# Kernel tuning notes

Hardware: AMD Instinct MI355X
Metric: run time of the kernel (lower is better)

The kernel has to match this reference:

```python
import jax, jax.numpy as jnp
import numpy as np

B, G, K, C, NT = 128, 64, 32, 256, 8192


def setup_inputs() -> dict:
    key = jax.random.key(0)
    ks = jax.random.split(key, 8)
    s = lambda fan_in: 1.0 / np.sqrt(fan_in)
    return {
        "patch_features": jax.random.normal(ks[0], (B, G, C), jnp.float32),
        "neighborhood": jax.random.normal(ks[1], (B, G, K, 3), jnp.float32),
        "codebook": jax.random.normal(ks[2], (NT, C), jnp.float32),
        "w1": jax.random.normal(ks[3], (512, C), jnp.float32) * s(C),
        "b1": jnp.zeros((512,), jnp.float32),
        "w2": jax.random.normal(ks[4], (256, 512), jnp.float32) * s(512),
        "b2": jnp.zeros((256,), jnp.float32),
        "w3": jax.random.normal(ks[5], (3 * K, 256), jnp.float32) * s(256),
        "b3": jnp.zeros((3 * K,), jnp.float32),
    }


def reference(patch_features, neighborhood, codebook, w1, b1, w2, b2, w3, b3):
    b, g, c = patch_features.shape
    k = neighborhood.shape[2]
    # squared euclidean distances to codebook (argmin equals argmin of cdist p=2)
    d2 = (
        jnp.sum(patch_features * patch_features, -1, keepdims=True)
        - 2.0 * jnp.einsum("bgc,nc->bgn", patch_features, codebook)
        + jnp.sum(codebook * codebook, -1)
    )  # [B,G,NT]
    token_ids = jnp.argmin(d2, axis=-1)          # [B,G]
    quantized = codebook[token_ids]              # [B,G,C] gather
    # 1x1 Conv1d stack == per-token MLP
    h = jax.nn.relu(jnp.einsum("bgc,oc->bgo", quantized, w1) + b1)
    h = jax.nn.relu(jnp.einsum("bgc,oc->bgo", h, w2) + b2)
    rec = jnp.einsum("bgc,oc->bgo", h, w3) + b3  # [B,G,3K]
    rec = rec.reshape(b * g, k, 3)
    gt = neighborhood.reshape(b * g, k, 3)
    # Chamfer distance L2 (squared) both directions
    diff = rec[:, :, None, :] - gt[:, None, :, :]  # [BG,K,K,3]
    dd = jnp.sum(diff * diff, -1)                  # [BG,K,K]
    loss = jnp.mean(jnp.min(dd, axis=2)) + jnp.mean(jnp.min(dd, axis=1))
    return loss
```

## Files before the change

kernel.cpp:

```cpp
#include <hip/hip_runtime.h>
#include <hip/hip_bf16.h>
#include <float.h>

#define NTOK 8192
#define NCB  8192
#define CDIM 256
#define KPTS 32
#define SQNT 24.0f
#define INV_CFOLD (SQNT * SQNT * 64.0f)

#define CG   4
#define NTPB 16

typedef __attribute__((ext_vector_type(8))) short short8;
typedef __attribute__((ext_vector_type(4))) float f32x4;
typedef __attribute__((ext_vector_type(4))) int i32x4;
typedef __attribute__((ext_vector_type(16))) int i32x16;
typedef unsigned int u32;
typedef unsigned long long u64;

__device__ __forceinline__ void gl_lds16(const void* g, void* l) {
  __builtin_amdgcn_global_load_lds(
      (const __attribute__((address_space(1))) u32*)(g),
      (__attribute__((address_space(3))) u32*)(l), 16, 0, 0);
}

__device__ __forceinline__ ushort bf16_rne(float x) {
  u32 u = __float_as_uint(x);
  return (ushort)((u + 0x7fffu + ((u >> 16) & 1u)) >> 16);
}

__device__ __forceinline__ int pack4i8(int a, int b, int c, int d) {
  return (a & 0xff) | ((b & 0xff) << 8) | ((c & 0xff) << 16) | ((d & 0xff) << 24);
}

__global__ __launch_bounds__(256) void prep_k(
    const float* __restrict__ pf, const float* __restrict__ cb,
    const float* __restrict__ w1, const float* __restrict__ w2,
    const float* __restrict__ w3,
    i32x4* __restrict__ pf1, i32x4* __restrict__ pf2,
    i32x4* __restrict__ cb1, i32x4* __restrict__ cb2,
    ushort* __restrict__ cb_bf, ushort* __restrict__ w1s,
    ushort* __restrict__ w2s, ushort* __restrict__ w3s,
    float* __restrict__ cnorm, float* __restrict__ out) {
  __shared__ float cred[4][16];
  if (blockIdx.x == 0 && threadIdx.x == 0) out[0] = 0.f;
  int gid = blockIdx.x * 4 + (threadIdx.x >> 6);
  int wv = threadIdx.x >> 6;
  int lane = threadIdx.x & 63, r16 = lane & 15, quad = lane >> 4;
  if (gid < 4096) {
    bool is_cb = gid >= 2048;
    int t = is_cb ? gid - 2048 : gid;
    int tile = t >> 2, kb = t & 3;
    const float* src = is_cb ? cb : pf;
    int row = tile * 16 + r16;
    const float* sp = src + (size_t)row * CDIM + kb * 64 + quad * 16;
    float4 v0 = ((const float4*)sp)[0];
    float4 v1 = ((const float4*)sp)[1];
    float4 v2 = ((const float4*)sp)[2];
    float4 v3 = ((const float4*)sp)[3];
    float x[16] = {v0.x, v0.y, v0.z, v0.w, v1.x, v1.y, v1.z, v1.w,
                   v2.x, v2.y, v2.z, v2.w, v3.x, v3.y, v3.z, v3.w};
    int q1[16], q2[16];
    float s = 0.f;
#pragma unroll
    for (int e = 0; e < 16; e++) {
      float as = x[e] * SQNT;
      float a1 = rintf(as);
      a1 = fminf(fmaxf(a1, -127.f), 127.f);
      float a2 = rintf((as - a1) * 128.f);
      a2 = fminf(fmaxf(a2, -127.f), 127.f);
      q1[e] = (int)a1;
      q2[e] = (int)a2;
      s += x[e] * x[e];
    }
    i32x4 p1 = {pack4i8(q1[0], q1[1], q1[2], q1[3]),
                pack4i8(q1[4], q1[5], q1[6], q1[7]),
                pack4i8(q1[8], q1[9], q1[10], q1[11]),
                pack4i8(q1[12], q1[13], q1[14], q1[15])};
    i32x4 p2 = {pack4i8(q2[0], q2[1], q2[2], q2[3]),
                pack4i8(q2[4], q2[5], q2[6], q2[7]),
                pack4i8(q2[8], q2[9], q2[10], q2[11]),
                pack4i8(q2[12], q2[13], q2[14], q2[15])};
    int rt32 = tile >> 1;
    int row_in = ((tile & 1) << 4) | r16;
    int kc32 = (kb << 1) | (quad >> 1);
    int k_half = quad & 1;
    size_t o = (size_t)(rt32 * 8 + kc32) * 64 + k_half * 32 + row_in;
    (is_cb ? cb1 : pf1)[o] = p1;
    (is_cb ? cb2 : pf2)[o] = p2;
    if (is_cb) {
      int kb32 = 2 * kb + (quad >> 1);
      int slot0 = ((2 * quad) & 3) * 16 + r16;
      int slot1 = ((2 * quad + 1) & 3) * 16 + r16;
      size_t bo = ((size_t)tile * 8 + kb32) * 512;
      short8 vh0 = {(short)bf16_rne(x[0]), (short)bf16_rne(x[1]),
                    (short)bf16_rne(x[2]), (short)bf16_rne(x[3]),
                    (short)bf16_rne(x[4]), (short)bf16_rne(x[5]),
                    (short)bf16_rne(x[6]), (short)bf16_rne(x[7])};
      short8 vh1 = {(short)bf16_rne(x[8]), (short)bf16_rne(x[9]),
                    (short)bf16_rne(x[10]), (short)bf16_rne(x[11]),
                    (short)bf16_rne(x[12]), (short)bf16_rne(x[13]),
                    (short)bf16_rne(x[14]), (short)bf16_rne(x[15])};
      *(short8*)(cb_bf + bo + (size_t)slot0 * 8) = vh0;
      *(short8*)(cb_bf + bo + (size_t)slot1 * 8) = vh1;
      s += __shfl_xor(s, 16, 64);
      s += __shfl_xor(s, 32, 64);
      if (quad == 0) cred[wv][r16] = s;
      __syncthreads();
      if (threadIdx.x < 16) {
        int ctile = blockIdx.x - 512;
        cnorm[ctile * 16 + threadIdx.x] =
            cred[0][threadIdx.x] + cred[1][threadIdx.x] +
            cred[2][threadIdx.x] + cred[3][threadIdx.x];
      }
    }
  } else if (gid < 4656) {
    int t = gid - 4096;
    const float* src;
    ushort* dst;
    int KB;
    if (t < 256)      { src = w1; dst = w1s; KB = 8; }
    else if (t < 512) { src = w2; dst = w2s; KB = 16; t -= 256; }
    else              { src = w3; dst = w3s; KB = 8;  t -= 512; }
    int tile = t / KB, kb = t - tile * KB, K = KB * 32;
    int row = tile * 16 + r16;
    const float* sp = src + (size_t)row * K + kb * 32 + quad * 8;
    float4 a = ((const float4*)sp)[0];
    float4 b = ((const float4*)sp)[1];
    short8 vh = {(short)bf16_rne(a.x), (short)bf16_rne(a.y),
                 (short)bf16_rne(a.z), (short)bf16_rne(a.w),
                 (short)bf16_rne(b.x), (short)bf16_rne(b.y),
                 (short)bf16_rne(b.z), (short)bf16_rne(b.w)};
    *(short8*)(dst + ((size_t)tile * KB + kb) * 512 + lane * 8) = vh;
  }
}

__device__ __forceinline__ void stage_b(const char* __restrict__ B1g,
                                        const char* __restrict__ B2g,
                                        size_t ctb, int kh, char* dst,
                                        int wv, int lane) {
#pragma unroll
  for (int u = 0; u < 8; ++u) {
    int c = wv * 8 + u;
    int lv = c >> 4, ct = (c >> 2) & 3, kc = (c & 3) + kh * 4;
    const char* src = (lv ? B2g : B1g) +
                      ((ctb + ct) * 8 + kc) * 1024 + (size_t)lane * 16;
    gl_lds16(src, dst + c * 1024);
  }
}

template <int KH>
__device__ __forceinline__ void phase_mfma(const char* bcur, int wc, int lane,
                                           const i32x4* a1, const i32x4* a2,
                                           i32x16* am, i32x16* ac) {
#pragma unroll
  for (int kk = 0; kk < 4; ++kk) {
#pragma unroll
    for (int j = 0; j < 2; ++j) {
      int ct = wc * 2 + j;
      i32x4 b1 = *(const i32x4*)(bcur + (ct * 4 + kk) * 1024 + lane * 16);
      i32x4 b2 = *(const i32x4*)(bcur + (16 + ct * 4 + kk) * 1024 + lane * 16);
      am[j] = __builtin_amdgcn_mfma_i32_32x32x32_i8(a1[KH * 4 + kk], b1, am[j], 0, 0, 0);
      ac[j] = __builtin_amdgcn_mfma_i32_32x32x32_i8(a1[KH * 4 + kk], b2, ac[j], 0, 0, 0);
      ac[j] = __builtin_amdgcn_mfma_i32_32x32x32_i8(a2[KH * 4 + kk], b1, ac[j], 0, 0, 0);
    }
  }
}

__global__ __launch_bounds__(256, 2) void argmin_k(
    const char* __restrict__ A1g, const char* __restrict__ A2g,
    const char* __restrict__ B1g, const char* __restrict__ B2g,
    const float* __restrict__ cnorm, u64* __restrict__ pkeys) {
  extern __shared__ char lds[];
  char* buf0 = lds;
  char* buf1 = lds + 32768;
  int tid = threadIdx.x;
  int cg = blockIdx.x, mt = blockIdx.y;
  int wv = tid >> 6, lane = tid & 63;
  int rt = wv >> 1, wc = wv & 1;
  int l31 = lane & 31, lh = lane >> 5;

  i32x4 a1[8], a2[8];
  {
    int rtg = mt * 2 + rt;
    const char* a1p = A1g + (size_t)rtg * 8192 + (size_t)lane * 16;
    const char* a2p = A2g + (size_t)rtg * 8192 + (size_t)lane * 16;
#pragma unroll
    for (int kc = 0; kc < 8; ++kc) {
      a1[kc] = *(const i32x4*)(a1p + kc * 1024);
      a2[kc] = *(const i32x4*)(a2p + kc * 1024);
    }
#pragma unroll
    for (int kc = 0; kc < 8; ++kc) {
      asm volatile("" : "+v"(a1[kc]));
      asm volatile("" : "+v"(a2[kc]));
    }
  }

  stage_b(B1g, B2g, (size_t)(cg * NTPB) * 4, 0, buf0, wv, lane);
  __syncthreads();

  int bvi[16], bii[16];
#pragma unroll
  for (int r = 0; r < 16; ++r) { bvi[r] = 0x7fffffff; bii[r] = 0x7fffffff; }

  i32x16 am[2], ac[2];

  for (int n = 0; n < NTPB; ++n) {
    size_t ctb = (size_t)(cg * NTPB + n) * 4;
    stage_b(B1g, B2g, ctb, 1, buf1, wv, lane);
#pragma unroll
    for (int j = 0; j < 2; ++j)
#pragma unroll
      for (int r = 0; r < 16; ++r) { am[j][r] = 0; ac[j][r] = 0; }
    phase_mfma<0>(buf0, wc, lane, a1, a2, am, ac);
    __syncthreads();
    if (n + 1 < NTPB) stage_b(B1g, B2g, ctb + 4, 0, buf0, wv, lane);
    phase_mfma<1>(buf1, wc, lane, a1, a2, am, ac);
    {
      int colbase = (cg * NTPB + n) * 128 + wc * 64;
#pragma unroll
      for (int j = 0; j < 2; ++j) {
        int col = colbase + j * 32 + l31;
        int cni = __float2int_rn(cnorm[col] * INV_CFOLD);
#pragma unroll
        for (int r = 0; r < 16; ++r) {
          int di = cni - (am[j][r] * 128 + ac[j][r]);
          if (di < bvi[r]) { bvi[r] = di; bii[r] = col; }
        }
      }
    }
    __syncthreads();
  }

#pragma unroll
  for (int m = 1; m < 32; m <<= 1) {
#pragma unroll
    for (int r = 0; r < 16; ++r) {
      int ov = __shfl_xor(bvi[r], m, 64);
      int oi = __shfl_xor(bii[r], m, 64);
      if (ov < bvi[r] || (ov == bvi[r] && oi < bii[r])) {
        bvi[r] = ov;
        bii[r] = oi;
      }
    }
  }
  if (l31 == 0) {
    int rowb = mt * 64 + rt * 32 + 4 * lh;
    size_t sbase = (size_t)(cg * 2 + wc) * NTOK;
#pragma unroll
    for (int r = 0; r < 16; ++r) {
      int row = rowb + (r & 3) + 8 * (r >> 2);
      u32 mk = (u32)(bvi[r] + (1 << 30));
      pkeys[sbase + row] = ((u64)mk << 32) | (u32)bii[r];
    }
  }
}

__global__ __launch_bounds__(512) void mlp_fused_k(
    const u64* __restrict__ pkeys, const ushort* __restrict__ cb_bf,
    const ushort* __restrict__ w1s, const float* __restrict__ b1,
    const ushort* __restrict__ w2s, const float* __restrict__ b2,
    const ushort* __restrict__ w3s, const float* __restrict__ b3,
    const float* __restrict__ neigh, float* __restrict__ out) {
  __shared__ ushort qs_h2[8 * 512];
  __shared__ ushort h1s[16 * 512];
  __shared__ float rec[16 * 96];
  __shared__ float gts[16 * 96];
  __shared__ int ids[16];
  __shared__ float wsum[8];

  int tid = threadIdx.x;
  int t0 = blockIdx.x * 16;
  int wv = tid >> 6, lane = tid & 63;
  int quad = lane >> 4, r16 = lane & 15;

  if (tid < 128) {
    int row_l = tid >> 3, sl = tid & 7;
    u64 best = pkeys[(size_t)sl * NTOK + t0 + row_l];
#pragma unroll
    for (int m = 1; m < 8; m <<= 1) {
      u64 o = __shfl_xor((unsigned long long)best, m, 64);
      if (o < best) best = o;
    }
    if (sl == 0) ids[row_l] = (int)(u32)best;
  }
  __syncthreads();

  {
    int kb = wv;
    int id = ids[r16];
    short8 v = *(const short8*)(cb_bf + ((size_t)(id >> 4) * 8 + kb) * 512 +
                                (size_t)((id & 15) + quad * 16) * 8);
    *(short8*)(qs_h2 + (size_t)kb * 512 + lane * 8) = v;
  }
  __syncthreads();

  short8 fa1[8];
#pragma unroll
  for (int kb = 0; kb < 8; kb++)
    fa1[kb] = *(const short8*)(qs_h2 + (size_t)kb * 512 + lane * 8);
  __syncthreads();

#pragma unroll
  for (int jj = 0; jj < 4; ++jj) {
    int jt = wv + jj * 8;
    f32x4 acc = (f32x4){0.f, 0.f, 0.f, 0.f};
#pragma unroll
    for (int kb = 0; kb < 8; kb++) {
      short8 fb = *(const short8*)(w1s + ((size_t)jt * 8 + kb) * 512 + lane * 8);
      acc = __builtin_amdgcn_mfma_f32_16x16x32_bf16(fa1[kb], fb, acc, 0, 0, 0);
    }
    int col = jt * 16 + r16;
    float bj = b1[col];
#pragma unroll
    for (int reg = 0; reg < 4; reg++) {
      int row_l = quad * 4 + reg;
      float v = fmaxf(acc[reg] + bj, 0.f);
      size_t o = (size_t)(col >> 5) * 512 +
                 (size_t)(((col >> 3) & 3) * 16 + row_l) * 8 + (col & 7);
      h1s[o] = bf16_rne(v);
    }
  }
  __syncthreads();

#pragma unroll
  for (int jj = 0; jj < 2; ++jj) {
    int jt = wv + jj * 8;
    f32x4 acc = (f32x4){0.f, 0.f, 0.f, 0.f};
#pragma unroll
    for (int kb = 0; kb < 16; kb++) {
      short8 fa = *(const short8*)(h1s + (size_t)kb * 512 + lane * 8);
      short8 fb = *(const short8*)(w2s + ((size_t)jt * 16 + kb) * 512 + lane * 8);
      acc = __builtin_amdgcn_mfma_f32_16x16x32_bf16(fa, fb, acc, 0, 0, 0);
    }
    int col = jt * 16 + r16;
    float bj = b2[col];
#pragma unroll
    for (int reg = 0; reg < 4; reg++) {
      int row_l = quad * 4 + reg;
      float v = fmaxf(acc[reg] + bj, 0.f);
      size_t o = (size_t)(col >> 5) * 512 +
                 (size_t)(((col >> 3) & 3) * 16 + row_l) * 8 + (col & 7);
      qs_h2[o] = bf16_rne(v);
    }
  }
  __syncthreads();

  if (tid < 384) {
    int t = tid / 24, c = (tid - t * 24) * 4;
    *(float4*)(gts + (size_t)t * 96 + c) =
        *(const float4*)(neigh + (size_t)(t0 + t) * 96 + c);
  }

  if (wv < 6) {
    int jt = wv;
    f32x4 acc = (f32x4){0.f, 0.f, 0.f, 0.f};
#pragma unroll
    for (int kb = 0; kb < 8; kb++) {
      short8 fa = *(const short8*)(qs_h2 + (size_t)kb * 512 + lane * 8);
      short8 fb = *(const short8*)(w3s + ((size_t)jt * 8 + kb) * 512 + lane * 8);
      acc = __builtin_amdgcn_mfma_f32_16x16x32_bf16(fa, fb, acc, 0, 0, 0);
    }
    int col = jt * 16 + r16;
    float bj = b3[col];
#pragma unroll
    for (int reg = 0; reg < 4; reg++) {
      int row_l = quad * 4 + reg;
      rec[(size_t)row_l * 96 + col] = acc[reg] + bj;
    }
  }
  __syncthreads();

  float local = 0.f;
  {
    int t = tid >> 5, i = tid & 31;
    float rx = rec[t * 96 + 3 * i], ry = rec[t * 96 + 3 * i + 1], rz = rec[t * 96 + 3 * i + 2];
    float gx = gts[t * 96 + 3 * i], gy = gts[t * 96 + 3 * i + 1], gz = gts[t * 96 + 3 * i + 2];
    float mA = FLT_MAX, mB = FLT_MAX;
#pragma unroll
    for (int j = 0; j < 32; j++) {
      float dx = rx - gts[t * 96 + 3 * j], dy = ry - gts[t * 96 + 3 * j + 1],
            dz = rz - gts[t * 96 + 3 * j + 2];
      float d = dx * dx + dy * dy + dz * dz;
      mA = fminf(mA, d);
      dx = rec[t * 96 + 3 * j] - gx; dy = rec[t * 96 + 3 * j + 1] - gy;
      dz = rec[t * 96 + 3 * j + 2] - gz;
      d = dx * dx + dy * dy + dz * dz;
      mB = fminf(mB, d);
    }
    local = mA + mB;
  }
#pragma unroll
  for (int off = 32; off; off >>= 1) local += __shfl_down(local, off, 64);
  if (lane == 0) wsum[wv] = local;
  __syncthreads();
  if (tid == 0) {
    float s = 0.f;
#pragma unroll
    for (int w = 0; w < 8; w++) s += wsum[w];
    atomicAdd(out, s * (1.0f / (float)(NTOK * KPTS)));
  }
}

extern "C" void kernel_launch(void* const* d_in, const int* in_sizes, int n_in,
                              void* d_out, int out_size, void* d_ws, size_t ws_size,
                              hipStream_t stream) {
  const float* pf    = (const float*)d_in[0];
  const float* neigh = (const float*)d_in[1];
  const float* cb    = (const float*)d_in[2];
  const float* w1    = (const float*)d_in[3];
  const float* b1    = (const float*)d_in[4];
  const float* w2    = (const float*)d_in[5];
  const float* b2    = (const float*)d_in[6];
  const float* w3    = (const float*)d_in[7];
  const float* b3    = (const float*)d_in[8];
  float* out = (float*)d_out;
  char* base = (char*)d_ws;

  u64*   pkeys = (u64*)base;
  float* cnorm = (float*)(base + 0x200000);
  char*  pf1   = base + 0x210000;
  char*  pf2   = base + 0x410000;
  char*  cb1   = base + 0x610000;
  char*  cb2   = base + 0x810000;
  ushort* cb_bf = (ushort*)(base + 0xA10000);
  ushort* w1s   = (ushort*)(base + 0xE10000);
  ushort* w2s   = (ushort*)(base + 0xE50000);
  ushort* w3s   = (ushort*)(base + 0xE90000);

  prep_k<<<1164, 256, 0, stream>>>(pf, cb, w1, w2, w3,
                                   (i32x4*)pf1, (i32x4*)pf2, (i32x4*)cb1,
                                   (i32x4*)cb2, cb_bf, w1s, w2s, w3s, cnorm, out);
  argmin_k<<<dim3(CG, 128), 256, 65536, stream>>>(pf1, pf2, cb1, cb2, cnorm, pkeys);
  mlp_fused_k<<<512, 512, 0, stream>>>(pkeys, cb_bf, w1s, b1, w2s, b2,
                                       w3s, b3, neigh, out);
}
```

Baseline: 162.8 us.

## Replace double-buffered B staging with 4-slot quarter-tile ring and vmcnt waits

Restructures the argmin GEMM's codebook staging from two 32KB halves with __syncthreads into a 4-slot ring of 16KB quarter-tiles, prefetched two phases ahead. It uses explicit s_waitcnt vmcnt counts with a single s_barrier per phase, so loads stay in flight across barriers instead of being fully drained. It also raises wave priority around the MFMA block. This trades finer-grained barriers (four per tile instead of two) and hand-tuned wait counts for better overlap of global-to-LDS copies with MFMA work.

Measured after the change: 164.5 us. Within noise of the previous version (+1.0%).

```diff
diff --git a/kernel.cpp b/kernel.cpp
--- a/kernel.cpp
+++ b/kernel.cpp
@@ -136,34 +136,70 @@
   }
 }
 
-__device__ __forceinline__ void stage_b(const char* __restrict__ B1g,
-                                        const char* __restrict__ B2g,
-                                        size_t ctb, int kh, char* dst,
-                                        int wv, int lane) {
-#pragma unroll
-  for (int u = 0; u < 8; ++u) {
-    int c = wv * 8 + u;
-    int lv = c >> 4, ct = (c >> 2) & 3, kc = (c & 3) + kh * 4;
-    const char* src = (lv ? B2g : B1g) +
-                      ((ctb + ct) * 8 + kc) * 1024 + (size_t)lane * 16;
-    gl_lds16(src, dst + c * 1024);
-  }
-}
-
-template <int KH>
-__device__ __forceinline__ void phase_mfma(const char* bcur, int wc, int lane,
-                                           const i32x4* a1, const i32x4* a2,
-                                           i32x16* am, i32x16* ac) {
-#pragma unroll
-  for (int kk = 0; kk < 4; ++kk) {
+__device__ __forceinline__ void stage_half(const char* __restrict__ B1g,
+                                           const char* __restrict__ B2g,
+                                           int cg, int G, char* dst,
+                                           int wv, int lane) {
+  int n_g = G >> 2, h_g = G & 3;
+  const char* base = ((wv & 2) ? B2g : B1g) +
+                     ((size_t)(cg * NTPB + n_g) << 15) + (size_t)lane * 16;
+#pragma unroll
+  for (int u = 0; u < 4; ++u) {
+    int ct = (wv & 1) * 2 + (u >> 1);
+    int kp = h_g * 2 + (u & 1);
+    int c  = (wv >> 1) * 8 + ct * 2 + (u & 1);
+    gl_lds16(base + ct * 8192 + kp * 1024, dst + c * 1024);
+  }
+}
+
+template <int HL, int VN, bool STG>
+__device__ __forceinline__ void phase(
+    const char* __restrict__ B1g, const char* __restrict__ B2g,
+    char* lds, int cg, int n, int wv, int wc, int lane, int l31,
+    const i32x4* a1, const i32x4* a2, i32x16* am, i32x16* ac,
+    const float* __restrict__ cnorm, int* bvi, int* bii) {
+  constexpr int SLOT = HL & 3;
+  constexpr int TSLOT = (HL + 2) & 3;
+  if constexpr (STG)
+    stage_half(B1g, B2g, cg, n * 4 + HL + 2, lds + TSLOT * 16384, wv, lane);
+  if constexpr (HL == 0) {
+#pragma unroll
+    for (int j = 0; j < 2; ++j)
+#pragma unroll
+      for (int r = 0; r < 16; ++r) { am[j][r] = 0; ac[j][r] = 0; }
+  }
+  if constexpr (VN == 8)      asm volatile("s_waitcnt vmcnt(8)" ::: "memory");
+  else if constexpr (VN == 4) asm volatile("s_waitcnt vmcnt(4)" ::: "memory");
+  else                        asm volatile("s_waitcnt vmcnt(0)" ::: "memory");
+  __builtin_amdgcn_s_barrier();
+  __builtin_amdgcn_sched_barrier(0);
+  const char* sb = lds + SLOT * 16384 + (size_t)lane * 16;
+  __builtin_amdgcn_s_setprio(1);
+#pragma unroll
+  for (int kcl = 0; kcl < 2; ++kcl) {
+    const int kp = HL * 2 + kcl;
 #pragma unroll
     for (int j = 0; j < 2; ++j) {
       int ct = wc * 2 + j;
-      i32x4 b1 = *(const i32x4*)(bcur + (ct * 4 + kk) * 1024 + lane * 16);
-      i32x4 b2 = *(const i32x4*)(bcur + (16 + ct * 4 + kk) * 1024 + lane * 16);
-      am[j] = __builtin_amdgcn_mfma_i32_32x32x32_i8(a1[KH * 4 + kk], b1, am[j], 0, 0, 0);
-      ac[j] = __builtin_amdgcn_mfma_i32_32x32x32_i8(a1[KH * 4 + kk], b2, ac[j], 0, 0, 0);
-      ac[j] = __builtin_amdgcn_mfma_i32_32x32x32_i8(a2[KH * 4 + kk], b1, ac[j], 0, 0, 0);
+      i32x4 b1 = *(const i32x4*)(sb + (ct * 2 + kcl) * 1024);
+      i32x4 b2 = *(const i32x4*)(sb + (8 + ct * 2 + kcl) * 1024);
+      am[j] = __builtin_amdgcn_mfma_i32_32x32x32_i8(a1[kp], b1, am[j], 0, 0, 0);
+      ac[j] = __builtin_amdgcn_mfma_i32_32x32x32_i8(a1[kp], b2, ac[j], 0, 0, 0);
+      ac[j] = __builtin_amdgcn_mfma_i32_32x32x32_i8(a2[kp], b1, ac[j], 0, 0, 0);
+    }
+  }
+  __builtin_amdgcn_s_setprio(0);
+  if constexpr (HL == 3) {
+    int colbase = (cg * NTPB + n) * 128 + wc * 64;
+#pragma unroll
+    for (int j = 0; j < 2; ++j) {
+      int col = colbase + j * 32 + l31;
+      int cni = __float2int_rn(cnorm[col] * INV_CFOLD);
+#pragma unroll
+      for (int r = 0; r < 16; ++r) {
+        int di = cni - (am[j][r] * 128 + ac[j][r]);
+        if (di < bvi[r]) { bvi[r] = di; bii[r] = col; }
+      }
     }
   }
 }
@@ -173,8 +209,6 @@
     const char* __restrict__ B1g, const char* __restrict__ B2g,
     const float* __restrict__ cnorm, u64* __restrict__ pkeys) {
   extern __shared__ char lds[];
-  char* buf0 = lds;
-  char* buf1 = lds + 32768;
   int tid = threadIdx.x;
   int cg = blockIdx.x, mt = blockIdx.y;
   int wv = tid >> 6, lane = tid & 63;
@@ -198,8 +232,8 @@
     }
   }
 
-  stage_b(B1g, B2g, (size_t)(cg * NTPB) * 4, 0, buf0, wv, lane);
-  __syncthreads();
+  stage_half(B1g, B2g, cg, 0, lds, wv, lane);
+  stage_half(B1g, B2g, cg, 1, lds + 16384, wv, lane);
 
   int bvi[16], bii[16];
 #pragma unroll
@@ -207,31 +241,18 @@
 
   i32x16 am[2], ac[2];
 
-  for (int n = 0; n < NTPB; ++n) {
-    size_t ctb = (size_t)(cg * NTPB + n) * 4;
-    stage_b(B1g, B2g, ctb, 1, buf1, wv, lane);
-#pragma unroll
-    for (int j = 0; j < 2; ++j)
-#pragma unroll
-      for (int r = 0; r < 16; ++r) { am[j][r] = 0; ac[j][r] = 0; }
-    phase_mfma<0>(buf0, wc, lane, a1, a2, am, ac);
-    __syncthreads();
-    if (n + 1 < NTPB) stage_b(B1g, B2g, ctb + 4, 0, buf0, wv, lane);
-    phase_mfma<1>(buf1, wc, lane, a1, a2, am, ac);
-    {
-      int colbase = (cg * NTPB + n) * 128 + wc * 64;
-#pragma unroll
-      for (int j = 0; j < 2; ++j) {
-        int col = colbase + j * 32 + l31;
-        int cni = __float2int_rn(cnorm[col] * INV_CFOLD);
-#pragma unroll
-        for (int r = 0; r < 16; ++r) {
-          int di = cni - (am[j][r] * 128 + ac[j][r]);
-          if (di < bvi[r]) { bvi[r] = di; bii[r] = col; }
-        }
-      }
-    }
-    __syncthreads();
+  for (int n = 0; n < NTPB - 1; ++n) {
+    phase<0, 8, true>(B1g, B2g, lds, cg, n, wv, wc, lane, l31, a1, a2, am, ac, cnorm, bvi, bii);
+    phase<1, 8, true>(B1g, B2g, lds, cg, n, wv, wc, lane, l31, a1, a2, am, ac, cnorm, bvi, bii);
+    phase<2, 8, true>(B1g, B2g, lds, cg, n, wv, wc, lane, l31, a1, a2, am, ac, cnorm, bvi, bii);
+    phase<3, 8, true>(B1g, B2g, lds, cg, n, wv, wc, lane, l31, a1, a2, am, ac, cnorm, bvi, bii);
+  }
+  {
+    const int n = NTPB - 1;
+    phase<0, 8, true >(B1g, B2g, lds, cg, n, wv, wc, lane, l31, a1, a2, am, ac, cnorm, bvi, bii);
+    phase<1, 8, true >(B1g, B2g, lds, cg, n, wv, wc, lane, l31, a1, a2, am, ac, cnorm, bvi, bii);
+    phase<2, 4, false>(B1g, B2g, lds, cg, n, wv, wc, lane, l31, a1, a2, am, ac, cnorm, bvi, bii);
+    phase<3, 0, false>(B1g, B2g, lds, cg, n, wv, wc, lane, l31, a1, a2, am, ac, cnorm, bvi, bii);
   }
 
 #pragma unroll
```

## Split argmin codebook across more blocks with narrower tiles and MFMA priority

Applied to the files above, without the earlier changes.

The codebook sweep is split into 16 column groups instead of 4. Each block now handles 64-column tiles instead of 128, so each wave keeps one accumulator pair rather than two. The LDS double buffer is halved, which allows three blocks per CU, and the MFMA loops are wrapped in s_setprio. The MLP kernel now reduces 32 partial argmin keys per token instead of 8. The aim is more blocks and more occupancy to hide load latency, at the cost of more partial-result writes and a larger final reduction.

Result: slower. 172.4 us (+5.9%).

```diff
diff --git a/kernel.cpp b/kernel.cpp
--- a/kernel.cpp
+++ b/kernel.cpp
@@ -9,8 +9,8 @@
 #define SQNT 24.0f
 #define INV_CFOLD (SQNT * SQNT * 64.0f)
 
-#define CG   4
-#define NTPB 16
+#define CG   16
+#define NTPB 8
 
 typedef __attribute__((ext_vector_type(8))) short short8;
 typedef __attribute__((ext_vector_type(4))) float f32x4;
@@ -136,45 +136,27 @@
   }
 }
 
-__device__ __forceinline__ void stage_b(const char* __restrict__ B1g,
-                                        const char* __restrict__ B2g,
-                                        size_t ctb, int kh, char* dst,
-                                        int wv, int lane) {
-#pragma unroll
-  for (int u = 0; u < 8; ++u) {
-    int c = wv * 8 + u;
-    int lv = c >> 4, ct = (c >> 2) & 3, kc = (c & 3) + kh * 4;
+__device__ __forceinline__ void stage_ph(const char* __restrict__ B1g,
+                                         const char* __restrict__ B2g,
+                                         int ctb , int kh,
+                                         char* dst, int wv, int lane) {
+#pragma unroll
+  for (int u = 0; u < 4; ++u) {
+    int c = wv * 4 + u;
+    int lv = c >> 3, ct = (c >> 2) & 1, kcl = c & 3;
     const char* src = (lv ? B2g : B1g) +
-                      ((ctb + ct) * 8 + kc) * 1024 + (size_t)lane * 16;
+        ((size_t)(ctb + ct) * 8 + kh * 4 + kcl) * 1024 + (size_t)lane * 16;
     gl_lds16(src, dst + c * 1024);
   }
 }
 
-template <int KH>
-__device__ __forceinline__ void phase_mfma(const char* bcur, int wc, int lane,
-                                           const i32x4* a1, const i32x4* a2,
-                                           i32x16* am, i32x16* ac) {
-#pragma unroll
-  for (int kk = 0; kk < 4; ++kk) {
-#pragma unroll
-    for (int j = 0; j < 2; ++j) {
-      int ct = wc * 2 + j;
-      i32x4 b1 = *(const i32x4*)(bcur + (ct * 4 + kk) * 1024 + lane * 16);
-      i32x4 b2 = *(const i32x4*)(bcur + (16 + ct * 4 + kk) * 1024 + lane * 16);
-      am[j] = __builtin_amdgcn_mfma_i32_32x32x32_i8(a1[KH * 4 + kk], b1, am[j], 0, 0, 0);
-      ac[j] = __builtin_amdgcn_mfma_i32_32x32x32_i8(a1[KH * 4 + kk], b2, ac[j], 0, 0, 0);
-      ac[j] = __builtin_amdgcn_mfma_i32_32x32x32_i8(a2[KH * 4 + kk], b1, ac[j], 0, 0, 0);
-    }
-  }
-}
-
-__global__ __launch_bounds__(256, 2) void argmin_k(
+__global__ __launch_bounds__(256, 3) void argmin_k(
     const char* __restrict__ A1g, const char* __restrict__ A2g,
     const char* __restrict__ B1g, const char* __restrict__ B2g,
     const float* __restrict__ cnorm, u64* __restrict__ pkeys) {
   extern __shared__ char lds[];
   char* buf0 = lds;
-  char* buf1 = lds + 32768;
+  char* buf1 = lds + 16384;
   int tid = threadIdx.x;
   int cg = blockIdx.x, mt = blockIdx.y;
   int wv = tid >> 6, lane = tid & 63;
@@ -198,37 +180,55 @@
     }
   }
 
-  stage_b(B1g, B2g, (size_t)(cg * NTPB) * 4, 0, buf0, wv, lane);
+  stage_ph(B1g, B2g, cg * NTPB * 2, 0, buf0, wv, lane);
   __syncthreads();
 
   int bvi[16], bii[16];
 #pragma unroll
   for (int r = 0; r < 16; ++r) { bvi[r] = 0x7fffffff; bii[r] = 0x7fffffff; }
 
-  i32x16 am[2], ac[2];
+  i32x16 am, ac;
 
   for (int n = 0; n < NTPB; ++n) {
-    size_t ctb = (size_t)(cg * NTPB + n) * 4;
-    stage_b(B1g, B2g, ctb, 1, buf1, wv, lane);
-#pragma unroll
-    for (int j = 0; j < 2; ++j)
-#pragma unroll
-      for (int r = 0; r < 16; ++r) { am[j][r] = 0; ac[j][r] = 0; }
-    phase_mfma<0>(buf0, wc, lane, a1, a2, am, ac);
+    int ctb = (cg * NTPB + n) * 2;
+    stage_ph(B1g, B2g, ctb, 1, buf1, wv, lane);
+#pragma unroll
+    for (int r = 0; r < 16; ++r) { am[r] = 0; ac[r] = 0; }
+    {
+      const char* sb = buf0 + (size_t)(wc * 4) * 1024 + (size_t)lane * 16;
+      __builtin_amdgcn_s_setprio(1);
+#pragma unroll
+      for (int kc = 0; kc < 4; ++kc) {
+        i32x4 b1 = *(const i32x4*)(sb + kc * 1024);
+        i32x4 b2 = *(const i32x4*)(sb + 8192 + kc * 1024);
+        am = __builtin_amdgcn_mfma_i32_32x32x32_i8(a1[kc], b1, am, 0, 0, 0);
+        ac = __builtin_amdgcn_mfma_i32_32x32x32_i8(a1[kc], b2, ac, 0, 0, 0);
+        ac = __builtin_amdgcn_mfma_i32_32x32x32_i8(a2[kc], b1, ac, 0, 0, 0);
+      }
+      __builtin_amdgcn_s_setprio(0);
+    }
     __syncthreads();
-    if (n + 1 < NTPB) stage_b(B1g, B2g, ctb + 4, 0, buf0, wv, lane);
-    phase_mfma<1>(buf1, wc, lane, a1, a2, am, ac);
+    if (n + 1 < NTPB) stage_ph(B1g, B2g, ctb + 2, 0, buf0, wv, lane);
     {
-      int colbase = (cg * NTPB + n) * 128 + wc * 64;
-#pragma unroll
-      for (int j = 0; j < 2; ++j) {
-        int col = colbase + j * 32 + l31;
-        int cni = __float2int_rn(cnorm[col] * INV_CFOLD);
-#pragma unroll
-        for (int r = 0; r < 16; ++r) {
-          int di = cni - (am[j][r] * 128 + ac[j][r]);
-          if (di < bvi[r]) { bvi[r] = di; bii[r] = col; }
-        }
+      const char* sb = buf1 + (size_t)(wc * 4) * 1024 + (size_t)lane * 16;
+      __builtin_amdgcn_s_setprio(1);
+#pragma unroll
+      for (int kc = 0; kc < 4; ++kc) {
+        i32x4 b1 = *(const i32x4*)(sb + kc * 1024);
+        i32x4 b2 = *(const i32x4*)(sb + 8192 + kc * 1024);
+        am = __builtin_amdgcn_mfma_i32_32x32x32_i8(a1[4 + kc], b1, am, 0, 0, 0);
+        ac = __builtin_amdgcn_mfma_i32_32x32x32_i8(a1[4 + kc], b2, ac, 0, 0, 0);
+        ac = __builtin_amdgcn_mfma_i32_32x32x32_i8(a2[4 + kc], b1, ac, 0, 0, 0);
+      }
+      __builtin_amdgcn_s_setprio(0);
+    }
+    {
+      int col = (cg * NTPB + n) * 64 + wc * 32 + l31;
+      int cni = __float2int_rn(cnorm[col] * INV_CFOLD);
+#pragma unroll
+      for (int r = 0; r < 16; ++r) {
+        int di = cni - (am[r] * 128 + ac[r]);
+        if (di < bvi[r]) { bvi[r] = di; bii[r] = col; }
       }
     }
     __syncthreads();
@@ -276,11 +276,11 @@
   int wv = tid >> 6, lane = tid & 63;
   int quad = lane >> 4, r16 = lane & 15;
 
-  if (tid < 128) {
-    int row_l = tid >> 3, sl = tid & 7;
+  {
+    int row_l = tid >> 5, sl = tid & 31;
     u64 best = pkeys[(size_t)sl * NTOK + t0 + row_l];
 #pragma unroll
-    for (int m = 1; m < 8; m <<= 1) {
+    for (int m = 1; m < 32; m <<= 1) {
       u64 o = __shfl_xor((unsigned long long)best, m, 64);
       if (o < best) best = o;
     }
@@ -433,7 +433,7 @@
   prep_k<<<1164, 256, 0, stream>>>(pf, cb, w1, w2, w3,
                                    (i32x4*)pf1, (i32x4*)pf2, (i32x4*)cb1,
                                    (i32x4*)cb2, cb_bf, w1s, w2s, w3s, cnorm, out);
-  argmin_k<<<dim3(CG, 128), 256, 65536, stream>>>(pf1, pf2, cb1, cb2, cnorm, pkeys);
+  argmin_k<<<dim3(CG, 128), 256, 32768, stream>>>(pf1, pf2, cb1, cb2, cnorm, pkeys);
   mlp_fused_k<<<512, 512, 0, stream>>>(pkeys, cb_bf, w1s, b1, w2s, b2,
                                        w3s, b3, neigh, out);
 }
```

## Stream codebook tiles directly into registers in argmin, dropping LDS staging

Applied to the files above, without the earlier changes.

Rewrites the int8 MFMA argmin kernel so each wave owns one 32-row token tile and loads codebook fragments straight from global memory into double-buffered registers. This replaces the shared-memory staging and the per-iteration block barriers. Codebook norms are now precomputed once per block into LDS, and the grid becomes 8 column groups by 64 row groups. The cost is that the four waves of a block each fetch the same codebook data separately, which raises L2/global traffic and makes the loop more sensitive to memory latency.

Measured after the change: 166.9 us. 1.02x slower.

```diff
diff --git a/kernel.cpp b/kernel.cpp
--- a/kernel.cpp
+++ b/kernel.cpp
@@ -9,8 +9,8 @@
 #define SQNT 24.0f
 #define INV_CFOLD (SQNT * SQNT * 64.0f)
 
-#define CG   4
-#define NTPB 16
+#define CG   8
+#define TW   32
 
 typedef __attribute__((ext_vector_type(8))) short short8;
 typedef __attribute__((ext_vector_type(4))) float f32x4;
@@ -18,12 +18,6 @@
 typedef __attribute__((ext_vector_type(16))) int i32x16;
 typedef unsigned int u32;
 typedef unsigned long long u64;
-
-__device__ __forceinline__ void gl_lds16(const void* g, void* l) {
-  __builtin_amdgcn_global_load_lds(
-      (const __attribute__((address_space(1))) u32*)(g),
-      (__attribute__((address_space(3))) u32*)(l), 16, 0, 0);
-}
 
 __device__ __forceinline__ ushort bf16_rne(float x) {
   u32 u = __float_as_uint(x);
@@ -136,35 +130,24 @@
   }
 }
 
-__device__ __forceinline__ void stage_b(const char* __restrict__ B1g,
-                                        const char* __restrict__ B2g,
-                                        size_t ctb, int kh, char* dst,
-                                        int wv, int lane) {
-#pragma unroll
-  for (int u = 0; u < 8; ++u) {
-    int c = wv * 8 + u;
-    int lv = c >> 4, ct = (c >> 2) & 3, kc = (c & 3) + kh * 4;
-    const char* src = (lv ? B2g : B1g) +
-                      ((ctb + ct) * 8 + kc) * 1024 + (size_t)lane * 16;
-    gl_lds16(src, dst + c * 1024);
-  }
-}
-
-template <int KH>
-__device__ __forceinline__ void phase_mfma(const char* bcur, int wc, int lane,
-                                           const i32x4* a1, const i32x4* a2,
-                                           i32x16* am, i32x16* ac) {
-#pragma unroll
-  for (int kk = 0; kk < 4; ++kk) {
-#pragma unroll
-    for (int j = 0; j < 2; ++j) {
-      int ct = wc * 2 + j;
-      i32x4 b1 = *(const i32x4*)(bcur + (ct * 4 + kk) * 1024 + lane * 16);
-      i32x4 b2 = *(const i32x4*)(bcur + (16 + ct * 4 + kk) * 1024 + lane * 16);
-      am[j] = __builtin_amdgcn_mfma_i32_32x32x32_i8(a1[KH * 4 + kk], b1, am[j], 0, 0, 0);
-      ac[j] = __builtin_amdgcn_mfma_i32_32x32x32_i8(a1[KH * 4 + kk], b2, ac[j], 0, 0, 0);
-      ac[j] = __builtin_amdgcn_mfma_i32_32x32x32_i8(a2[KH * 4 + kk], b1, ac[j], 0, 0, 0);
-    }
+__device__ __forceinline__ void loadh(const char* bb1, const char* bb2,
+                                      int offb, i32x4 (&q1)[4], i32x4 (&q2)[4]) {
+#pragma unroll
+  for (int k = 0; k < 4; ++k) {
+    q1[k] = *(const i32x4*)(bb1 + (size_t)(offb + k) * 1024);
+    q2[k] = *(const i32x4*)(bb2 + (size_t)(offb + k) * 1024);
+  }
+}
+
+template <int KB>
+__device__ __forceinline__ void mfmah(const i32x4* a1, const i32x4* a2,
+                                      const i32x4 (&q1)[4], const i32x4 (&q2)[4],
+                                      i32x16& am, i32x16& ac) {
+#pragma unroll
+  for (int k = 0; k < 4; ++k) {
+    am = __builtin_amdgcn_mfma_i32_32x32x32_i8(a1[KB + k], q1[k], am, 0, 0, 0);
+    ac = __builtin_amdgcn_mfma_i32_32x32x32_i8(a1[KB + k], q2[k], ac, 0, 0, 0);
+    ac = __builtin_amdgcn_mfma_i32_32x32x32_i8(a2[KB + k], q1[k], ac, 0, 0, 0);
   }
 }
 
@@ -172,18 +155,18 @@
     const char* __restrict__ A1g, const char* __restrict__ A2g,
     const char* __restrict__ B1g, const char* __restrict__ B2g,
     const float* __restrict__ cnorm, u64* __restrict__ pkeys) {
-  extern __shared__ char lds[];
-  char* buf0 = lds;
-  char* buf1 = lds + 32768;
+  __shared__ int cni_lds[1024];
   int tid = threadIdx.x;
   int cg = blockIdx.x, mt = blockIdx.y;
   int wv = tid >> 6, lane = tid & 63;
-  int rt = wv >> 1, wc = wv & 1;
   int l31 = lane & 31, lh = lane >> 5;
+
+  for (int k = tid; k < 1024; k += 256)
+    cni_lds[k] = __float2int_rn(cnorm[cg * 1024 + k] * INV_CFOLD);
 
   i32x4 a1[8], a2[8];
   {
-    int rtg = mt * 2 + rt;
+    int rtg = mt * 4 + wv;
     const char* a1p = A1g + (size_t)rtg * 8192 + (size_t)lane * 16;
     const char* a2p = A2g + (size_t)rtg * 8192 + (size_t)lane * 16;
 #pragma unroll
@@ -197,41 +180,49 @@
       asm volatile("" : "+v"(a2[kc]));
     }
   }
-
-  stage_b(B1g, B2g, (size_t)(cg * NTPB) * 4, 0, buf0, wv, lane);
   __syncthreads();
 
   int bvi[16], bii[16];
 #pragma unroll
   for (int r = 0; r < 16; ++r) { bvi[r] = 0x7fffffff; bii[r] = 0x7fffffff; }
 
-  i32x16 am[2], ac[2];
-
-  for (int n = 0; n < NTPB; ++n) {
-    size_t ctb = (size_t)(cg * NTPB + n) * 4;
-    stage_b(B1g, B2g, ctb, 1, buf1, wv, lane);
-#pragma unroll
-    for (int j = 0; j < 2; ++j)
-#pragma unroll
-      for (int r = 0; r < 16; ++r) { am[j][r] = 0; ac[j][r] = 0; }
-    phase_mfma<0>(buf0, wc, lane, a1, a2, am, ac);
-    __syncthreads();
-    if (n + 1 < NTPB) stage_b(B1g, B2g, ctb + 4, 0, buf0, wv, lane);
-    phase_mfma<1>(buf1, wc, lane, a1, a2, am, ac);
-    {
-      int colbase = (cg * NTPB + n) * 128 + wc * 64;
-#pragma unroll
-      for (int j = 0; j < 2; ++j) {
-        int col = colbase + j * 32 + l31;
-        int cni = __float2int_rn(cnorm[col] * INV_CFOLD);
-#pragma unroll
-        for (int r = 0; r < 16; ++r) {
-          int di = cni - (am[j][r] * 128 + ac[j][r]);
-          if (di < bvi[r]) { bvi[r] = di; bii[r] = col; }
-        }
-      }
-    }
-    __syncthreads();
+  const char* bb1 = B1g + (size_t)(cg * TW) * 8192 + (size_t)lane * 16;
+  const char* bb2 = B2g + (size_t)(cg * TW) * 8192 + (size_t)lane * 16;
+
+  i32x4 q1A[4], q2A[4], q1B[4], q2B[4];
+  i32x16 am, ac;
+
+  loadh(bb1, bb2, 0, q1A, q2A);
+  loadh(bb1, bb2, 4, q1B, q2B);
+
+  for (int t = 0; t < TW - 1; ++t) {
+#pragma unroll
+    for (int r = 0; r < 16; ++r) { am[r] = 0; ac[r] = 0; }
+    mfmah<0>(a1, a2, q1A, q2A, am, ac);
+    loadh(bb1, bb2, (t + 1) * 8, q1A, q2A);
+    mfmah<4>(a1, a2, q1B, q2B, am, ac);
+    loadh(bb1, bb2, (t + 1) * 8 + 4, q1B, q2B);
+    int cni = cni_lds[t * 32 + l31];
+    int col = cg * 1024 + t * 32 + l31;
+#pragma unroll
+    for (int r = 0; r < 16; ++r) {
+      int di = cni - (am[r] * 128 + ac[r]);
+      if (di < bvi[r]) { bvi[r] = di; bii[r] = col; }
+    }
+  }
+  {
+    const int t = TW - 1;
+#pragma unroll
+    for (int r = 0; r < 16; ++r) { am[r] = 0; ac[r] = 0; }
+    mfmah<0>(a1, a2, q1A, q2A, am, ac);
+    mfmah<4>(a1, a2, q1B, q2B, am, ac);
+    int cni = cni_lds[t * 32 + l31];
+    int col = cg * 1024 + t * 32 + l31;
+#pragma unroll
+    for (int r = 0; r < 16; ++r) {
+      int di = cni - (am[r] * 128 + ac[r]);
+      if (di < bvi[r]) { bvi[r] = di; bii[r] = col; }
+    }
   }
 
 #pragma unroll
@@ -247,8 +238,8 @@
     }
   }
   if (l31 == 0) {
-    int rowb = mt * 64 + rt * 32 + 4 * lh;
-    size_t sbase = (size_t)(cg * 2 + wc) * NTOK;
+    int rowb = mt * 128 + wv * 32 + 4 * lh;
+    size_t sbase = (size_t)cg * NTOK;
 #pragma unroll
     for (int r = 0; r < 16; ++r) {
       int row = rowb + (r & 3) + 8 * (r >> 2);
@@ -433,7 +424,7 @@
   prep_k<<<1164, 256, 0, stream>>>(pf, cb, w1, w2, w3,
                                    (i32x4*)pf1, (i32x4*)pf2, (i32x4*)cb1,
                                    (i32x4*)cb2, cb_bf, w1s, w2s, w3s, cnorm, out);
-  argmin_k<<<dim3(CG, 128), 256, 65536, stream>>>(pf1, pf2, cb1, cb2, cnorm, pkeys);
+  argmin_k<<<dim3(CG, 64), 256, 0, stream>>>(pf1, pf2, cb1, cb2, cnorm, pkeys);
   mlp_fused_k<<<512, 512, 0, stream>>>(pkeys, cb_bf, w1s, b1, w2s, b2,
                                        w3s, b3, neigh, out);
 }
```
